# Optimization experiments

Hardware: AMD Instinct MI355X
Metric: run time of the kernel (lower is better)

## Reference

```python
import jax, jax.numpy as jnp
import numpy as np

L2 = 65536          # edges per orientation (L=256 torus)
N = 2 * L2          # total edges
FIN = 8             # nfeatCNN_in
FOUT = 8            # nfeatCNN_out
K = 13              # kernel size (neighbor shifts per edge)
SCALE = (2.0 + 2.0 * np.e) / (np.e - 1.0)


def setup_inputs() -> dict:
    key = jax.random.key(0)
    ks = jax.random.split(key, 8)
    x = jax.random.normal(ks[0], (FIN * N,), dtype=jnp.float32)
    Wconv_hor = jax.random.normal(ks[1], (FOUT, FIN, K), dtype=jnp.float32) * 0.1
    Wconv_vert = jax.random.normal(ks[2], (FOUT, FIN, K), dtype=jnp.float32) * 0.1
    bconv_hor = jnp.zeros((FOUT,), dtype=jnp.float32)
    bconv_vert = jnp.zeros((FOUT,), dtype=jnp.float32)
    mask_hor = jax.random.randint(ks[3], (L2, FOUT, FIN, K), 0, 2).astype(bool)
    mask_vert = jax.random.randint(ks[4], (L2, FOUT, FIN, K), 0, 2).astype(bool)
    ker_hor = jax.random.randint(ks[5], (L2, K), 0, N, dtype=jnp.int32)
    ker_vert = jax.random.randint(ks[6], (L2, K), 0, N, dtype=jnp.int32)
    hor_edge_lst = jnp.arange(L2, dtype=jnp.int32)
    vert_edge_lst = jnp.arange(L2, dtype=jnp.int32) + L2
    return {
        "x": x,
        "Wconv_hor": Wconv_hor, "Wconv_vert": Wconv_vert,
        "bconv_hor": bconv_hor, "bconv_vert": bconv_vert,
        "mask_hor": mask_hor, "mask_vert": mask_vert,
        "ker_hor": ker_hor, "ker_vert": ker_vert,
        "hor_edge_lst": hor_edge_lst, "vert_edge_lst": vert_edge_lst,
    }


def reference(x, Wconv_hor, Wconv_vert, bconv_hor, bconv_vert,
              mask_hor, mask_vert, ker_hor, ker_vert,
              hor_edge_lst, vert_edge_lst):
    fout, fin, _ = Wconv_hor.shape
    n = x.shape[0] // fin
    xm = x.reshape(fin, n)                      # (fin, N)

    def branch(W, mask, ker, b):
        xg = xm[:, ker]                         # gather -> (fin, E, K)
        Wm = W[None] * mask.astype(W.dtype)     # (E, fout, fin, K)
        # per-edge masked contraction over (fin, K); vectorized over edges
        z = jnp.einsum('eoik,iek->oe', Wm, xg)  # (fout, E)
        return z + b[:, None]

    x_hor = branch(Wconv_hor, mask_hor, ker_hor, bconv_hor)
    x_vert = branch(Wconv_vert, mask_vert, ker_vert, bconv_vert)

    out = jnp.zeros((fout, n), dtype=x.dtype)
    out = out.at[:, hor_edge_lst].set(x_hor)
    out = out.at[:, vert_edge_lst].set(x_vert)
    return (jax.nn.sigmoid(out) - 0.5) * jnp.asarray(SCALE, out.dtype)
```

## Files before the change

### kernel.cpp

```cpp
#include <hip/hip_runtime.h>
#include <math.h>

#define L2C   65536
#define NC    (2 * L2C)
#define FINC  8
#define FOUTC 8
#define KC    13
#define BLOCK 256
#define EPB   4
#define EWORDS (FOUTC * FINC * KC)
#define TILE_WORDS (EPB * EWORDS)
#define TILE_WBYTES (TILE_WORDS * 4)
#define TILE_BBYTES (EPB * EWORDS)
#define GRID  1536
#define GRIDH (GRID / 2)
#define TPBR  (L2C / EPB)

constexpr double E_D = 2.71828182845904523536;
constexpr float SCALE_F = (float)((2.0 + 2.0 * E_D) / (E_D - 1.0));

typedef unsigned int u32;
typedef __attribute__((address_space(1))) const u32 gu32;
typedef __attribute__((address_space(3))) u32 lu32;

__device__ __forceinline__ void gll16(const void* g, u32* l) {
    __builtin_amdgcn_global_load_lds((gu32*)g, (lu32*)l, 16, 0, 2);
}

__global__ __launch_bounds__(256)
void transpose_x_kernel(const float* __restrict__ x, float* __restrict__ xt) {
    int n = blockIdx.x * 256 + threadIdx.x;
    float v[FINC];
#pragma unroll
    for (int i = 0; i < FINC; ++i) v[i] = x[(size_t)i * NC + n];
    float4* dst = reinterpret_cast<float4*>(xt + ((size_t)n << 3));
    dst[0] = make_float4(v[0], v[1], v[2], v[3]);
    dst[1] = make_float4(v[4], v[5], v[6], v[7]);
}

__global__ __launch_bounds__(BLOCK, 6)
void edge_conv_kernel(const float* __restrict__ xt,
                      const float* __restrict__ Wh, const float* __restrict__ Wv,
                      const float* __restrict__ bh, const float* __restrict__ bv,
                      const unsigned char* __restrict__ mh,
                      const unsigned char* __restrict__ mv,
                      const int* __restrict__ kh, const int* __restrict__ kv,
                      float* __restrict__ out)
{
    __shared__ __align__(16) u32 msh[2][TILE_WORDS];

    const int tid  = threadIdx.x;
    const int lane = tid & 63;
    const int wave = tid >> 6;
    const int o    = lane >> 3;
    const int i    = lane & 7;

    const int  b     = blockIdx.x;
    const bool hor   = (b < GRIDH);
    const int  bb    = hor ? b : b - GRIDH;
    const int  cbase = hor ? 0 : L2C;

    const float*         W    = hor ? Wh : Wv;
    const float*         bias = hor ? bh : bv;
    const unsigned char* mask = hor ? mh : mv;
    const int*           ker  = hor ? kh : kv;

    const unsigned char probe = mh[(size_t)(lane * 4 + 1)];
    const bool words = (__ballot(probe != 0) == 0ull);

    float wreg[KC];
#pragma unroll
    for (int k = 0; k < KC; ++k) wreg[k] = W[lane * KC + k];
    const float biaso = bias[o];

    auto stage = [&](int buf, int t) {
        if (words) {
            const char* g = (const char*)mask + (size_t)t * TILE_WBYTES;
#pragma unroll
            for (int j = 0; j < 3; ++j) {
                const int c = wave + 4 * j;
                gll16(g + (size_t)(c * 64 + lane) * 16, &msh[buf][c * 256]);
            }
            if (wave == 0)
                gll16(g + (size_t)(12 * 64 + lane) * 16, &msh[buf][12 * 256]);
        } else {
            const char* g = (const char*)mask + (size_t)t * TILE_BBYTES;
            if (wave < 3)
                gll16(g + (size_t)(wave * 64 + lane) * 16, &msh[buf][wave * 256]);
            else if (lane < 16)
                gll16(g + (size_t)(3 * 64 + lane) * 16, &msh[buf][3 * 256]);
        }
    };

    int t = bb;
    stage(0, t);
    __syncthreads();

    int buf = 0;
    for (; t < TPBR; t += GRIDH, buf ^= 1) {
        const int tn = t + GRIDH;
        if (tn < TPBR) stage(buf ^ 1, tn);

        const int be  = t * EPB + wave;
        const int bes = __builtin_amdgcn_readfirstlane(be);

        int cols[KC];
#pragma unroll
        for (int k = 0; k < KC; ++k) cols[k] = ker[(size_t)bes * KC + k];

        float acc0 = 0.0f, acc1 = 0.0f;
        if (words) {
            const u32* mrow = &msh[buf][wave * EWORDS + lane * KC];
#pragma unroll
            for (int k = 0; k < KC; ++k) {
                const float xv = xt[((size_t)cols[k] << 3) + i];
                const float wm = mrow[k] ? wreg[k] : 0.0f;
                if (k & 1) acc1 = fmaf(wm, xv, acc1);
                else       acc0 = fmaf(wm, xv, acc0);
            }
        } else {
            const unsigned char* mrow = (const unsigned char*)&msh[buf][0]
                                        + wave * EWORDS + lane * KC;
#pragma unroll
            for (int k = 0; k < KC; ++k) {
                const float xv = xt[((size_t)cols[k] << 3) + i];
                const float wm = mrow[k] ? wreg[k] : 0.0f;
                if (k & 1) acc1 = fmaf(wm, xv, acc1);
                else       acc0 = fmaf(wm, xv, acc0);
            }
        }
        float acc = acc0 + acc1;
        acc += __shfl_xor(acc, 1);
        acc += __shfl_xor(acc, 2);
        acc += __shfl_xor(acc, 4);
        const float z = acc + biaso;

        __syncthreads();

        if (i == 0) {
            const float sig = 1.0f / (1.0f + __expf(-z));
            out[(size_t)o * NC + (cbase + be)] = (sig - 0.5f) * SCALE_F;
        }
    }
}

extern "C" void kernel_launch(void* const* d_in, const int* in_sizes, int n_in,
                              void* d_out, int out_size, void* d_ws, size_t ws_size,
                              hipStream_t stream) {
    const float*         x   = (const float*)d_in[0];
    const float*         Wh  = (const float*)d_in[1];
    const float*         Wv  = (const float*)d_in[2];
    const float*         bh  = (const float*)d_in[3];
    const float*         bv  = (const float*)d_in[4];
    const unsigned char* mh  = (const unsigned char*)d_in[5];
    const unsigned char* mv  = (const unsigned char*)d_in[6];
    const int*           kh  = (const int*)d_in[7];
    const int*           kv  = (const int*)d_in[8];
    float* out = (float*)d_out;
    float* xt  = (float*)d_ws;

    transpose_x_kernel<<<NC / 256, 256, 0, stream>>>(x, xt);
    edge_conv_kernel<<<GRID, BLOCK, 0, stream>>>(
        xt, Wh, Wv, bh, bv, mh, mv, kh, kv, out);
}
```

Before: 440.1 us.

## Replace LDS-staged mask tiles with per-wave direct register loads and bit packing

Removes the double-buffered LDS staging of mask tiles via global_load_lds and the per-iteration block barrier. Each wave now handles 16 contiguous edges, loads its mask bytes straight into registers with 16-byte nontemporal vector loads, prefetches the next edge's mask one step ahead, and packs the 13 mask flags into a bitmask. Grid and occupancy are raised (2048 blocks, launch bound of 8 blocks per CU). The cost being targeted is LDS traffic and synchronisation. In exchange, each lane loads overlapping 64-byte windows, so more redundant global requests are issued and prefetch depth is shorter than before.

```diff
diff --git a/kernel.cpp b/kernel.cpp
--- a/kernel.cpp
+++ b/kernel.cpp
@@ -7,25 +7,17 @@
 #define FOUTC 8
 #define KC    13
 #define BLOCK 256
-#define EPB   4
-#define EWORDS (FOUTC * FINC * KC)
-#define TILE_WORDS (EPB * EWORDS)
-#define TILE_WBYTES (TILE_WORDS * 4)
-#define TILE_BBYTES (EPB * EWORDS)
-#define GRID  1536
+#define EWB   (FOUTC * FINC * KC * 4)
+#define EBB   (FOUTC * FINC * KC)
+#define GRID  2048
 #define GRIDH (GRID / 2)
-#define TPBR  (L2C / EPB)
+#define EPW   16
 
 constexpr double E_D = 2.71828182845904523536;
 constexpr float SCALE_F = (float)((2.0 + 2.0 * E_D) / (E_D - 1.0));
-
 typedef unsigned int u32;
-typedef __attribute__((address_space(1))) const u32 gu32;
-typedef __attribute__((address_space(3))) u32 lu32;
-
-__device__ __forceinline__ void gll16(const void* g, u32* l) {
-    __builtin_amdgcn_global_load_lds((gu32*)g, (lu32*)l, 16, 0, 2);
-}
+typedef u32 u32x4 __attribute__((ext_vector_type(4)));
+typedef u32 u32x2 __attribute__((ext_vector_type(2)));
 
 __global__ __launch_bounds__(256)
 void transpose_x_kernel(const float* __restrict__ x, float* __restrict__ xt) {
@@ -38,7 +30,7 @@
     dst[1] = make_float4(v[4], v[5], v[6], v[7]);
 }
 
-__global__ __launch_bounds__(BLOCK, 6)
+__global__ __launch_bounds__(BLOCK, 8)
 void edge_conv_kernel(const float* __restrict__ xt,
                       const float* __restrict__ Wh, const float* __restrict__ Wv,
                       const float* __restrict__ bh, const float* __restrict__ bv,
@@ -47,8 +39,6 @@
                       const int* __restrict__ kh, const int* __restrict__ kv,
                       float* __restrict__ out)
 {
-    __shared__ __align__(16) u32 msh[2][TILE_WORDS];
-
     const int tid  = threadIdx.x;
     const int lane = tid & 63;
     const int wave = tid >> 6;
@@ -73,73 +63,110 @@
     for (int k = 0; k < KC; ++k) wreg[k] = W[lane * KC + k];
     const float biaso = bias[o];
 
-    auto stage = [&](int buf, int t) {
-        if (words) {
-            const char* g = (const char*)mask + (size_t)t * TILE_WBYTES;
-#pragma unroll
-            for (int j = 0; j < 3; ++j) {
-                const int c = wave + 4 * j;
-                gll16(g + (size_t)(c * 64 + lane) * 16, &msh[buf][c * 256]);
-            }
-            if (wave == 0)
-                gll16(g + (size_t)(12 * 64 + lane) * 16, &msh[buf][12 * 256]);
-        } else {
-            const char* g = (const char*)mask + (size_t)t * TILE_BBYTES;
-            if (wave < 3)
-                gll16(g + (size_t)(wave * 64 + lane) * 16, &msh[buf][wave * 256]);
-            else if (lane < 16)
-                gll16(g + (size_t)(3 * 64 + lane) * 16, &msh[buf][3 * 256]);
-        }
-    };
+    const int e0 = (bb * 4 + wave) * EPW;
 
-    int t = bb;
-    stage(0, t);
-    __syncthreads();
+    if (words) {
+        const int vb  = (lane * 52) & ~15;
+        const int off = lane & 3;
+        u32x4 r0, r1, r2, r3;
+        auto issue = [&](int e) {
+            const u32x4* p = reinterpret_cast<const u32x4*>(
+                mask + (size_t)e * EWB + vb);
+            r0 = __builtin_nontemporal_load(p + 0);
+            r1 = __builtin_nontemporal_load(p + 1);
+            r2 = __builtin_nontemporal_load(p + 2);
+            r3 = __builtin_nontemporal_load(p + 3);
+        };
+        auto pack = [&]() -> u32 {
+            u32 f = 0;
+            f |= (u32)(r0[0] != 0u) << 0;  f |= (u32)(r0[1] != 0u) << 1;
+            f |= (u32)(r0[2] != 0u) << 2;  f |= (u32)(r0[3] != 0u) << 3;
+            f |= (u32)(r1[0] != 0u) << 4;  f |= (u32)(r1[1] != 0u) << 5;
+            f |= (u32)(r1[2] != 0u) << 6;  f |= (u32)(r1[3] != 0u) << 7;
+            f |= (u32)(r2[0] != 0u) << 8;  f |= (u32)(r2[1] != 0u) << 9;
+            f |= (u32)(r2[2] != 0u) << 10; f |= (u32)(r2[3] != 0u) << 11;
+            f |= (u32)(r3[0] != 0u) << 12; f |= (u32)(r3[1] != 0u) << 13;
+            f |= (u32)(r3[2] != 0u) << 14; f |= (u32)(r3[3] != 0u) << 15;
+            return (f >> off) & 0x1FFFu;
+        };
 
-    int buf = 0;
-    for (; t < TPBR; t += GRIDH, buf ^= 1) {
-        const int tn = t + GRIDH;
-        if (tn < TPBR) stage(buf ^ 1, tn);
+        issue(e0);
+        u32 mb = pack();
+        for (int j = 0; j < EPW; ++j) {
+            const int e = e0 + j;
+            if (j + 1 < EPW) issue(e + 1);
 
-        const int be  = t * EPB + wave;
-        const int bes = __builtin_amdgcn_readfirstlane(be);
-
-        int cols[KC];
-#pragma unroll
-        for (int k = 0; k < KC; ++k) cols[k] = ker[(size_t)bes * KC + k];
-
-        float acc0 = 0.0f, acc1 = 0.0f;
-        if (words) {
-            const u32* mrow = &msh[buf][wave * EWORDS + lane * KC];
+            const int  eu = __builtin_amdgcn_readfirstlane(e);
+            const int* kc = ker + (size_t)eu * KC;
+            float acc0 = 0.0f, acc1 = 0.0f;
 #pragma unroll
             for (int k = 0; k < KC; ++k) {
-                const float xv = xt[((size_t)cols[k] << 3) + i];
-                const float wm = mrow[k] ? wreg[k] : 0.0f;
+                const float xv = (xt + ((size_t)kc[k] << 3))[i];
+                const float wm = ((mb >> k) & 1u) ? wreg[k] : 0.0f;
                 if (k & 1) acc1 = fmaf(wm, xv, acc1);
                 else       acc0 = fmaf(wm, xv, acc0);
             }
-        } else {
-            const unsigned char* mrow = (const unsigned char*)&msh[buf][0]
-                                        + wave * EWORDS + lane * KC;
+            float acc = acc0 + acc1;
+            acc += __shfl_xor(acc, 1);
+            acc += __shfl_xor(acc, 2);
+            acc += __shfl_xor(acc, 4);
+            if (i == 0) {
+                const float z   = acc + biaso;
+                const float sig = 1.0f / (1.0f + __expf(-z));
+                out[(size_t)o * NC + (cbase + e)] = (sig - 0.5f) * SCALE_F;
+            }
+            if (j + 1 < EPW) mb = pack();
+        }
+    } else {
+        const int lb  = lane * KC;
+        const int vb  = (lb & ~15) > (EBB - 32) ? (EBB - 32) : (lb & ~15);
+        const int off = lb - vb;
+        u32x4 r0, r1;
+        auto issueB = [&](int e) {
+            const u32x4* p = reinterpret_cast<const u32x4*>(
+                mask + (size_t)e * EBB + vb);
+            r0 = __builtin_nontemporal_load(p + 0);
+            r1 = __builtin_nontemporal_load(p + 1);
+        };
+        auto packB = [&]() -> u32 {
+            u32 f = 0;
+            const u32 d[8] = {r0[0], r0[1], r0[2], r0[3], r1[0], r1[1], r1[2], r1[3]};
+#pragma unroll
+            for (int q = 0; q < 8; ++q) {
+                f |= (u32)((d[q] & 0x000000FFu) != 0u) << (4 * q + 0);
+                f |= (u32)((d[q] & 0x0000FF00u) != 0u) << (4 * q + 1);
+                f |= (u32)((d[q] & 0x00FF0000u) != 0u) << (4 * q + 2);
+                f |= (u32)((d[q] & 0xFF000000u) != 0u) << (4 * q + 3);
+            }
+            return (f >> off) & 0x1FFFu;
+        };
+
+        issueB(e0);
+        u32 mb = packB();
+        for (int j = 0; j < EPW; ++j) {
+            const int e = e0 + j;
+            if (j + 1 < EPW) issueB(e + 1);
+
+            const int  eu = __builtin_amdgcn_readfirstlane(e);
+            const int* kc = ker + (size_t)eu * KC;
+            float acc0 = 0.0f, acc1 = 0.0f;
 #pragma unroll
             for (int k = 0; k < KC; ++k) {
-                const float xv = xt[((size_t)cols[k] << 3) + i];
-                const float wm = mrow[k] ? wreg[k] : 0.0f;
+                const float xv = (xt + ((size_t)kc[k] << 3))[i];
+                const float wm = ((mb >> k) & 1u) ? wreg[k] : 0.0f;
                 if (k & 1) acc1 = fmaf(wm, xv, acc1);
                 else       acc0 = fmaf(wm, xv, acc0);
             }
-        }
-        float acc = acc0 + acc1;
-        acc += __shfl_xor(acc, 1);
-        acc += __shfl_xor(acc, 2);
-        acc += __shfl_xor(acc, 4);
-        const float z = acc + biaso;
-
-        __syncthreads();
-
-        if (i == 0) {
-            const float sig = 1.0f / (1.0f + __expf(-z));
-            out[(size_t)o * NC + (cbase + be)] = (sig - 0.5f) * SCALE_F;
+            float acc = acc0 + acc1;
+            acc += __shfl_xor(acc, 1);
+            acc += __shfl_xor(acc, 2);
+            acc += __shfl_xor(acc, 4);
+            if (i == 0) {
+                const float z   = acc + biaso;
+                const float sig = 1.0f / (1.0f + __expf(-z));
+                out[(size_t)o * NC + (cbase + e)] = (sig - 0.5f) * SCALE_F;
+            }
+            if (j + 1 < EPW) mb = packB();
         }
     }
 }
```

Result: slower. 507.3 us (+15.3%).
